# Kernel tuning notes

Hardware: AMD Instinct MI355X
Metric: run time of the kernel (lower is better)

## Reference

```python
import jax, jax.numpy as jnp
import numpy as np

BATCH, SEQ_LEN, D_MODEL, STATE_DIM = 8, 4096, 512, 64
LN_EPS = 1e-5


def _hippo_log_neg_eigs(state_dim):
    A = np.zeros((state_dim, state_dim))
    for i in range(state_dim):
        for j in range(state_dim):
            if i > j:
                A[i, j] = -((2 * i + 1) ** 0.5) * ((2 * j + 1) ** 0.5)
            elif i == j:
                A[i, j] = -(i + 1)
    ev = np.sort(np.linalg.eigvals(A).real)[:state_dim]
    return np.log(-ev + 1e-06).astype(np.float32)


def setup_inputs() -> dict:
    key = jax.random.key(0)
    ks = jax.random.split(key, 8)
    d, s = D_MODEL, STATE_DIM
    return {
        "x": jax.random.normal(ks[0], (BATCH, SEQ_LEN, d), dtype=jnp.float32),
        "log_A": jnp.asarray(_hippo_log_neg_eigs(s)),
        "B": jax.random.normal(ks[1], (d, s), dtype=jnp.float32) * 0.01,
        "C": jax.random.normal(ks[2], (s, d), dtype=jnp.float32) * 0.01,
        "D": jnp.zeros((d,), dtype=jnp.float32),
        "log_dt": jnp.zeros((), dtype=jnp.float32),
        "gamma": jnp.ones((d,), dtype=jnp.float32),
        "beta": jnp.zeros((d,), dtype=jnp.float32),
        "W1": jax.random.normal(ks[3], (d, 2 * d), dtype=jnp.float32) * (1.0 / np.sqrt(d)),
        "b1": jnp.zeros((2 * d,), dtype=jnp.float32),
        "W2": jax.random.normal(ks[4], (2 * d, d), dtype=jnp.float32) * (1.0 / np.sqrt(2 * d)),
        "b2": jnp.zeros((d,), dtype=jnp.float32),
    }


def _layernorm(x, gamma, beta):
    mu = jnp.mean(x, axis=-1, keepdims=True)
    var = jnp.mean(jnp.square(x - mu), axis=-1, keepdims=True)
    return (x - mu) * jax.lax.rsqrt(var + LN_EPS) * gamma + beta


def reference(x, log_A, B, C, D, log_dt, gamma, beta, W1, b1, W2, b2):
    residual = x
    xn = _layernorm(x, gamma, beta)  # [B, L, D]

    dt = jnp.exp(log_dt)
    A_bar = jnp.exp(-jnp.exp(log_A) * dt)  # [S]

    # Precompute input projections for all timesteps, then scan the diagonal recurrence.
    xB = jnp.einsum("bld,ds->lbs", xn, B)  # [L, B, S]
    h0 = jnp.zeros((xn.shape[0], A_bar.shape[0]), dtype=xn.dtype)

    def step(h, xb_t):
        h = A_bar * h + xb_t
        return h, h

    _, hs = jax.lax.scan(step, h0, xB)  # hs: [L, B, S]

    y = jnp.einsum("lbs,sd->bld", hs, C) + xn * D  # [B, L, D]
    y = y + residual

    yn = _layernorm(y, gamma, beta)
    mlp = jax.nn.gelu(yn @ W1 + b1, approximate=False) @ W2 + b2
    return y + mlp
```

## Files before the change

kernel.cpp:

```cpp
#include <hip/hip_runtime.h>
#include <math.h>

#define BATCH 8
#define SEQL 4096
#define DMODEL 512
#define SDIM 64
#define MROWS (BATCH * SEQL)
#define LN_EPS 1e-5f

typedef __attribute__((ext_vector_type(8))) short bf16x8;
typedef __attribute__((ext_vector_type(4))) float f32x4;

__device__ __forceinline__ float wave_sum(float v) {
#pragma unroll
  for (int off = 32; off > 0; off >>= 1) v += __shfl_xor(v, off, 64);
  return v;
}

__device__ __forceinline__ unsigned short f2bf(float f) {
  unsigned int u = __float_as_uint(f);
  u += 0x7fffu + ((u >> 16) & 1u);
  return (unsigned short)(u >> 16);
}

__device__ __forceinline__ float gelu_fast(float v) {
  float s = v * 0.70710678118654752f;
  float ax = fabsf(s);
  float t = 1.0f / (1.0f + 0.3275911f * ax);
  float p = ((((1.061405429f * t - 1.453152027f) * t + 1.421413741f) * t - 0.284496736f) * t +
             0.254829592f) *
            t;
  float er = 1.0f - p * __expf(-ax * ax);
  er = copysignf(er, s);
  return 0.5f * v * (1.0f + er);
}

__device__ __forceinline__ void gl2lds16(const void* g, void* l) {
  __builtin_amdgcn_global_load_lds((const __attribute__((address_space(1))) void*)g,
                                   (__attribute__((address_space(3))) void*)l, 16, 0, 0);
}

__global__ void ln_stats_kernel(const float* __restrict__ x, float* __restrict__ mu,
                                float* __restrict__ rstd, unsigned short* __restrict__ xbf) {
  int row = blockIdx.x * 4 + (threadIdx.x >> 6);
  int lane = threadIdx.x & 63;
  const float4* xp = (const float4*)(x + (size_t)row * DMODEL);
  float4 a = xp[lane * 2];
  float4 b = xp[lane * 2 + 1];
  float s = a.x + a.y + a.z + a.w + b.x + b.y + b.z + b.w;
  float q = a.x * a.x + a.y * a.y + a.z * a.z + a.w * a.w + b.x * b.x + b.y * b.y +
            b.z * b.z + b.w * b.w;
  s = wave_sum(s);
  q = wave_sum(q);
  uint4 pk;
  pk.x = (unsigned)f2bf(a.x) | ((unsigned)f2bf(a.y) << 16);
  pk.y = (unsigned)f2bf(a.z) | ((unsigned)f2bf(a.w) << 16);
  pk.z = (unsigned)f2bf(b.x) | ((unsigned)f2bf(b.y) << 16);
  pk.w = (unsigned)f2bf(b.z) | ((unsigned)f2bf(b.w) << 16);
  ((uint4*)(xbf + (size_t)row * DMODEL))[lane] = pk;
  if (lane == 0) {
    float m = s * (1.0f / DMODEL);
    float var = q * (1.0f / DMODEL) - m * m;
    mu[row] = m;
    rstd[row] = rsqrtf(var + LN_EPS);
  }
}

__device__ __forceinline__ void transpose_body(const float* __restrict__ W,
                                               unsigned short* __restrict__ Wt, int K, int N,
                                               int bx, int by,
                                               unsigned short (*tile)[65]) {
  int k0 = by * 64, n0 = bx * 64;
  int tx = threadIdx.x & 15, ty = threadIdx.x >> 4;
#pragma unroll
  for (int p = 0; p < 4; ++p) {
    int k = p * 16 + ty;
    float4 v = *(const float4*)&W[(size_t)(k0 + k) * N + n0 + tx * 4];
    tile[tx * 4 + 0][k] = f2bf(v.x);
    tile[tx * 4 + 1][k] = f2bf(v.y);
    tile[tx * 4 + 2][k] = f2bf(v.z);
    tile[tx * 4 + 3][k] = f2bf(v.w);
  }
  __syncthreads();
#pragma unroll
  for (int p = 0; p < 4; ++p) {
    int n = p * 16 + ty;
    ushort4 o;
    o.x = tile[n][tx * 4 + 0];
    o.y = tile[n][tx * 4 + 1];
    o.z = tile[n][tx * 4 + 2];
    o.w = tile[n][tx * 4 + 3];
    *(ushort4*)&Wt[(size_t)(n0 + n) * K + k0 + tx * 4] = o;
  }
}

__global__ __launch_bounds__(256) void prep_all_kernel(
    const float* __restrict__ W1, const float* __restrict__ W2, const float* __restrict__ Cm,
    const float* __restrict__ Bm, const float* __restrict__ gamma,
    const float* __restrict__ beta, unsigned short* __restrict__ w1t,
    unsigned short* __restrict__ w2t, unsigned short* __restrict__ ctb,
    unsigned short* __restrict__ Bgt, float* __restrict__ gB, float* __restrict__ bB) {
  __shared__ unsigned short tile[64][65];
  int b = blockIdx.x;
  if (b < 128) {
    transpose_body(W1, w1t, 512, 1024, b & 15, b >> 4, tile);
  } else if (b < 256) {
    transpose_body(W2, w2t, 1024, 512, (b - 128) & 7, (b - 128) >> 3, tile);
  } else if (b < 264) {
    transpose_body(Cm, ctb, 64, 512, b - 256, 0, tile);
  } else {
    int s = (b - 264) * 4 + (threadIdx.x >> 6);
    int l = threadIdx.x & 63;
    float gs = 0.0f, bs = 0.0f;
    unsigned short tmp[8];
#pragma unroll
    for (int u = 0; u < 8; ++u) {
      int d = l * 8 + u;
      float bv = Bm[(size_t)d * SDIM + s];
      float gv = gamma[d], ev = beta[d];
      gs += gv * bv;
      bs += ev * bv;
      tmp[u] = f2bf(gv * bv);
    }
    *(ushort4*)&Bgt[(size_t)s * DMODEL + l * 8] = make_ushort4(tmp[0], tmp[1], tmp[2], tmp[3]);
    *(ushort4*)&Bgt[(size_t)s * DMODEL + l * 8 + 4] =
        make_ushort4(tmp[4], tmp[5], tmp[6], tmp[7]);
    gs = wave_sum(gs);
    bs = wave_sum(bs);
    if (l == 0) {
      gB[s] = gs;
      bB[s] = bs;
    }
  }
}

__global__ __launch_bounds__(256) void xb_mfma_kernel(
    const unsigned short* __restrict__ xbf, const unsigned short* __restrict__ Bgt,
    const float* __restrict__ mu, const float* __restrict__ rstd, const float* __restrict__ gB,
    const float* __restrict__ bB, float* __restrict__ xB) {
  __shared__ unsigned short As[128 * 32];
  __shared__ unsigned short Bs[64 * 32];
  const int t = threadIdx.x;
  const int wave = t >> 6, lane = t & 63;
  const int m0 = blockIdx.x * 128;
  const int wm = wave * 32;
  const int row = t >> 2, seg = t & 3;
  const int fr = lane & 15, fq = lane >> 4;
  f32x4 acc[2][4] = {};
  for (int k0 = 0; k0 < DMODEL; k0 += 32) {
    __syncthreads();
    gl2lds16(xbf + (size_t)(m0 + row) * DMODEL + k0 + seg * 8, As + (size_t)(wave * 16) * 32);
    gl2lds16(xbf + (size_t)(m0 + 64 + row) * DMODEL + k0 + seg * 8,
             As + (size_t)(64 + wave * 16) * 32);
    gl2lds16(Bgt + (size_t)row * DMODEL + k0 + seg * 8, Bs + (size_t)(wave * 16) * 32);
    __syncthreads();
#pragma unroll
    for (int i = 0; i < 2; ++i) {
      bf16x8 a = *(const bf16x8*)&As[(wm + i * 16 + fr) * 32 + fq * 8];
#pragma unroll
      for (int j = 0; j < 4; ++j) {
        bf16x8 b = *(const bf16x8*)&Bs[(j * 16 + fr) * 32 + fq * 8];
        acc[i][j] = __builtin_amdgcn_mfma_f32_16x16x32_bf16(a, b, acc[i][j], 0, 0, 0);
      }
    }
  }
#pragma unroll
  for (int i = 0; i < 2; ++i)
#pragma unroll
    for (int r = 0; r < 4; ++r) {
      const int m = m0 + wm + i * 16 + fq * 4 + r;
      const float rr = rstd[m], negmurr = -mu[m] * rstd[m];
#pragma unroll
      for (int j = 0; j < 4; ++j) {
        const int s = j * 16 + fr;
        xB[(size_t)m * SDIM + s] = rr * acc[i][j][r] + negmurr * gB[s] + bB[s];
      }
    }
}

__global__ void scan_ends_kernel(const float* __restrict__ xB, const float* __restrict__ logA,
                                 const float* __restrict__ logdt, float* __restrict__ ends) {
  int t = blockIdx.x * 256 + threadIdx.x;
  int s = t & 63;
  int c = (t >> 6) & 63;
  int b = t >> 12;
  float a = expf(-expf(logA[s]) * expf(logdt[0]));
  const float* p = xB + ((size_t)(b * SEQL + c * 64)) * SDIM + s;
  float e = 0.0f;
#pragma unroll
  for (int i = 0; i < 64; ++i) e = a * e + p[(size_t)i * SDIM];
  ends[(b * 64 + c) * 64 + s] = e;
}

__global__ void scan_fix_kernel(const float* __restrict__ logA, const float* __restrict__ logdt,
                                const float* __restrict__ ends, const float* __restrict__ xB,
                                unsigned short* __restrict__ hsb) {
  int t = blockIdx.x * 256 + threadIdx.x;
  int s = t & 63;
  int c = (t >> 6) & 63;
  int b = t >> 12;
  float a = expf(-expf(logA[s]) * expf(logdt[0]));
  float a64 = a;
#pragma unroll
  for (int i = 0; i < 6; ++i) a64 *= a64;
  float h = 0.0f;
  for (int cp = 0; cp < c; ++cp) h = a64 * h + ends[(b * 64 + cp) * 64 + s];
  const float* p = xB + ((size_t)(b * SEQL + c * 64)) * SDIM + s;
  unsigned short* q = hsb + ((size_t)(b * SEQL + c * 64)) * SDIM + s;
#pragma unroll
  for (int i = 0; i < 64; ++i) {
    h = a * h + p[(size_t)i * SDIM];
    q[(size_t)i * SDIM] = f2bf(h);
  }
}

__global__ __launch_bounds__(256) void y_gemm_mfma_kernel(
    const unsigned short* __restrict__ hsb, const unsigned short* __restrict__ ctb,
    const float* __restrict__ x, const float* __restrict__ mu1,
    const float* __restrict__ rstd1, const float* __restrict__ gamma,
    const float* __restrict__ beta, const float* __restrict__ Dv, float* __restrict__ out) {
  __shared__ unsigned short As[2 * 128 * 32];
  __shared__ unsigned short Bs[2 * 128 * 32];
  const int t = threadIdx.x;
  const int w = t >> 6, lane = t & 63;
  const int m0 = blockIdx.y * 128, n0 = blockIdx.x * 128;
  const int wm = (w >> 1) * 64, wn = (w & 1) * 64;
  const int fr = lane & 15, fq = lane >> 4;
  const int srow = t >> 2, sseg = t & 3;
#pragma unroll
  for (int h = 0; h < 2; ++h)
#pragma unroll
    for (int c = 0; c < 2; ++c) {
      gl2lds16(hsb + (size_t)(m0 + c * 64 + srow) * SDIM + h * 32 + sseg * 8,
               As + ((size_t)h * 128 + c * 64 + w * 16) * 32);
      gl2lds16(ctb + (size_t)(n0 + c * 64 + srow) * SDIM + h * 32 + sseg * 8,
               Bs + ((size_t)h * 128 + c * 64 + w * 16) * 32);
    }
  __syncthreads();
  f32x4 acc[4][4] = {};
#pragma unroll
  for (int h = 0; h < 2; ++h) {
    bf16x8 a[4], b[4];
#pragma unroll
    for (int i = 0; i < 4; ++i)
      a[i] = *(const bf16x8*)&As[((size_t)h * 128 + wm + i * 16 + fr) * 32 + fq * 8];
#pragma unroll
    for (int j = 0; j < 4; ++j)
      b[j] = *(const bf16x8*)&Bs[((size_t)h * 128 + wn + j * 16 + fr) * 32 + fq * 8];
#pragma unroll
    for (int i = 0; i < 4; ++i)
#pragma unroll
      for (int j = 0; j < 4; ++j)
        acc[i][j] = __builtin_amdgcn_mfma_f32_16x16x32_bf16(a[i], b[j], acc[i][j], 0, 0, 0);
  }
  float mm[4][4], rr[4][4];
#pragma unroll
  for (int i = 0; i < 4; ++i)
#pragma unroll
    for (int r = 0; r < 4; ++r) {
      int m = m0 + wm + i * 16 + fq * 4 + r;
      mm[i][r] = mu1[m];
      rr[i][r] = rstd1[m];
    }
#pragma unroll
  for (int j = 0; j < 4; ++j) {
    const int n = n0 + wn + j * 16 + fr;
    const float ga = gamma[n], be = beta[n], dd = Dv[n];
#pragma unroll
    for (int i = 0; i < 4; ++i) {
      float xv[4];
#pragma unroll
      for (int r = 0; r < 4; ++r)
        xv[r] = x[(size_t)(m0 + wm + i * 16 + fq * 4 + r) * DMODEL + n];
#pragma unroll
      for (int r = 0; r < 4; ++r) {
        float yv = acc[i][j][r] + ((xv[r] - mm[i][r]) * rr[i][r] * ga + be) * dd + xv[r];
        out[(size_t)(m0 + wm + i * 16 + fq * 4 + r) * DMODEL + n] = yv;
      }
    }
  }
}

__global__ void ln_apply_kernel(const float* __restrict__ y, const float* __restrict__ gamma,
                                const float* __restrict__ beta,
                                unsigned short* __restrict__ yn) {
  int row = blockIdx.x * 4 + (threadIdx.x >> 6);
  int lane = threadIdx.x & 63;
  const float4* yp = (const float4*)(y + (size_t)row * DMODEL);
  float4 a = yp[lane * 2];
  float4 b = yp[lane * 2 + 1];
  float s = a.x + a.y + a.z + a.w + b.x + b.y + b.z + b.w;
  float q = a.x * a.x + a.y * a.y + a.z * a.z + a.w * a.w + b.x * b.x + b.y * b.y +
            b.z * b.z + b.w * b.w;
  s = wave_sum(s);
  q = wave_sum(q);
  float m = s * (1.0f / DMODEL);
  float var = q * (1.0f / DMODEL) - m * m;
  float rs = rsqrtf(var + LN_EPS);
  const float4* gp = (const float4*)gamma;
  const float4* bp = (const float4*)beta;
  float4 g0 = gp[lane * 2], g1 = gp[lane * 2 + 1];
  float4 e0 = bp[lane * 2], e1 = bp[lane * 2 + 1];
  float o0x = (a.x - m) * rs * g0.x + e0.x, o0y = (a.y - m) * rs * g0.y + e0.y;
  float o0z = (a.z - m) * rs * g0.z + e0.z, o0w = (a.w - m) * rs * g0.w + e0.w;
  float o1x = (b.x - m) * rs * g1.x + e1.x, o1y = (b.y - m) * rs * g1.y + e1.y;
  float o1z = (b.z - m) * rs * g1.z + e1.z, o1w = (b.w - m) * rs * g1.w + e1.w;
  uint4 pk;
  pk.x = (unsigned)f2bf(o0x) | ((unsigned)f2bf(o0y) << 16);
  pk.y = (unsigned)f2bf(o0z) | ((unsigned)f2bf(o0w) << 16);
  pk.z = (unsigned)f2bf(o1x) | ((unsigned)f2bf(o1y) << 16);
  pk.w = (unsigned)f2bf(o1z) | ((unsigned)f2bf(o1w) << 16);
  ((uint4*)(yn + (size_t)row * DMODEL))[lane] = pk;
}

template <int K, int NALL, int EPI>
__global__ __launch_bounds__(512, 2) void gemm256_kernel(
    const unsigned short* __restrict__ Am, const unsigned short* __restrict__ Bm,
    const float* __restrict__ bias, unsigned short* __restrict__ gout,
    float* __restrict__ out) {
  __shared__ alignas(16) unsigned short As[2][256 * 64];
  __shared__ alignas(16) unsigned short Bs[2][256 * 64];
  const int t = threadIdx.x;
  const int wid = t >> 6, lane = t & 63;
  const int m0 = blockIdx.y * 256, n0 = blockIdx.x * 256;
  const int wm = (wid >> 2) * 128, wn = (wid & 3) * 64;
  const int fr = lane & 15, fq = lane >> 4;
  constexpr int NT = K / 64;
  const int srow = t >> 3;
  const int ksw = ((t & 7) ^ ((t >> 3) & 7)) << 3;

  auto stageA = [&](int bb, int h, int kt) {
    const unsigned short* s0 = Am + (size_t)(m0 + h * 128 + srow) * K + kt * 64 + ksw;
    gl2lds16(s0, &As[bb][(h * 128 + wid * 8) * 64]);
    gl2lds16(s0 + (size_t)64 * K, &As[bb][(h * 128 + 64 + wid * 8) * 64]);
  };
  auto stageB = [&](int bb, int h, int kt) {
    const unsigned short* s0 = Bm + (size_t)(n0 + h * 128 + srow) * K + kt * 64 + ksw;
    gl2lds16(s0, &Bs[bb][(h * 128 + wid * 8) * 64]);
    gl2lds16(s0 + (size_t)64 * K, &Bs[bb][(h * 128 + 64 + wid * 8) * 64]);
  };
  auto LDA = [&](int bb, int i, int s) -> bf16x8 {
    const int row = wm + i * 16 + fr;
    const int slot = (s * 4 + fq) ^ (fr & 7);
    return *(const bf16x8*)&As[bb][row * 64 + slot * 8];
  };
  auto LDB = [&](int bb, int j, int s) -> bf16x8 {
    const int col = wn + j * 16 + fr;
    const int slot = (s * 4 + fq) ^ (fr & 7);
    return *(const bf16x8*)&Bs[bb][col * 64 + slot * 8];
  };

  stageA(0, 0, 0);
  stageA(0, 1, 0);
  stageB(0, 0, 0);
  stageB(0, 1, 0);
  stageB(1, 0, 1);
  stageB(1, 1, 1);
  asm volatile("s_waitcnt vmcnt(4)" ::: "memory");
  asm volatile("s_barrier" ::: "memory");

  f32x4 acc[8][4] = {};
  for (int c = 0; c < NT; ++c) {
    const int b = c & 1;
    bf16x8 bfr[2][4];
#pragma unroll
    for (int q = 0; q < 4; ++q) {
      bf16x8 a2[2][2];
#pragma unroll
      for (int ii = 0; ii < 2; ++ii)
#pragma unroll
        for (int s = 0; s < 2; ++s) a2[ii][s] = LDA(b, 2 * q + ii, s);
      if (q == 0) {
#pragma unroll
        for (int s = 0; s < 2; ++s)
#pragma unroll
          for (int j = 0; j < 4; ++j) bfr[s][j] = LDB(b, j, s);
        if (c + 1 < NT) stageA(b ^ 1, 0, c + 1);
      } else if (q == 1) {
        if (c + 1 < NT) stageA(b ^ 1, 1, c + 1);
      } else if (q == 2) {
        asm volatile("" ::: "memory");
        if (c + 2 < NT) stageB(b, 0, c + 2);
      } else {
        if (c + 2 < NT) stageB(b, 1, c + 2);
      }
      asm volatile("s_barrier" ::: "memory");
      __builtin_amdgcn_s_setprio(1);
#pragma unroll
      for (int ii = 0; ii < 2; ++ii)
#pragma unroll
        for (int s = 0; s < 2; ++s)
#pragma unroll
          for (int j = 0; j < 4; ++j)
            acc[2 * q + ii][j] = __builtin_amdgcn_mfma_f32_16x16x32_bf16(
                a2[ii][s], bfr[s][j], acc[2 * q + ii][j], 0, 0, 0);
      __builtin_amdgcn_s_setprio(0);
      if (q < 3) {
        asm volatile("s_barrier" ::: "memory");
      } else if (c < NT - 1) {
        if (c < NT - 2)
          asm volatile("s_waitcnt vmcnt(4)" ::: "memory");
        else
          asm volatile("s_waitcnt vmcnt(0)" ::: "memory");
        asm volatile("s_barrier" ::: "memory");
      }
    }
  }

#pragma unroll
  for (int i = 0; i < 8; ++i)
#pragma unroll
    for (int j = 0; j < 4; ++j) {
      const int cg = n0 + wn + j * 16 + fr;
      const float bb = bias[cg];
#pragma unroll
      for (int r = 0; r < 4; ++r) {
        const int rg = m0 + wm + i * 16 + fq * 4 + r;
        if (EPI == 0) {
          gout[(size_t)rg * NALL + cg] = f2bf(gelu_fast(acc[i][j][r] + bb));
        } else {
          const size_t off = (size_t)rg * NALL + cg;
          out[off] = out[off] + acc[i][j][r] + bb;
        }
      }
    }
}

extern "C" void kernel_launch(void* const* d_in, const int* in_sizes, int n_in, void* d_out,
                              int out_size, void* d_ws, size_t ws_size, hipStream_t stream) {
  const float* x = (const float*)d_in[0];
  const float* logA = (const float*)d_in[1];
  const float* Bm = (const float*)d_in[2];
  const float* Cm = (const float*)d_in[3];
  const float* Dv = (const float*)d_in[4];
  const float* logdt = (const float*)d_in[5];
  const float* gamma = (const float*)d_in[6];
  const float* beta = (const float*)d_in[7];
  const float* W1 = (const float*)d_in[8];
  const float* b1 = (const float*)d_in[9];
  const float* W2 = (const float*)d_in[10];
  const float* b2 = (const float*)d_in[11];
  float* out = (float*)d_out;

  char* ws = (char*)d_ws;
  float* mu1 = (float*)(ws + 0);
  float* rstd1 = (float*)(ws + 131072);
  float* ends = (float*)(ws + 262144);
  float* gB = (float*)(ws + 524288);
  float* bB = (float*)(ws + 524800);
  unsigned short* Bgt = (unsigned short*)(ws + 525312);
  unsigned short* ctb = (unsigned short*)(ws + 590848);
  unsigned short* w1t = (unsigned short*)(ws + 656384);
  unsigned short* w2t = (unsigned short*)(ws + 1704960);
  unsigned short* g = (unsigned short*)(ws + 2753536);
  unsigned short* xbf = (unsigned short*)(ws + 2753536);
  float* xB = (float*)(ws + 69862400);
  unsigned short* hsb = (unsigned short*)(ws + 78251008);
  unsigned short* yn = (unsigned short*)(ws + 82445312);

  prep_all_kernel<<<280, 256, 0, stream>>>(W1, W2, Cm, Bm, gamma, beta, w1t, w2t, ctb, Bgt, gB,
                                           bB);
  ln_stats_kernel<<<MROWS / 4, 256, 0, stream>>>(x, mu1, rstd1, xbf);
  xb_mfma_kernel<<<MROWS / 128, 256, 0, stream>>>(xbf, Bgt, mu1, rstd1, gB, bB, xB);
  scan_ends_kernel<<<128, 256, 0, stream>>>(xB, logA, logdt, ends);
  scan_fix_kernel<<<128, 256, 0, stream>>>(logA, logdt, ends, xB, hsb);
  y_gemm_mfma_kernel<<<dim3(DMODEL / 128, MROWS / 128), 256, 0, stream>>>(
      hsb, ctb, x, mu1, rstd1, gamma, beta, Dv, out);
  ln_apply_kernel<<<MROWS / 4, 256, 0, stream>>>(out, gamma, beta, yn);
  gemm256_kernel<512, 1024, 0><<<dim3(1024 / 256, MROWS / 256), 512, 0, stream>>>(
      yn, w1t, b1, g, nullptr);
  gemm256_kernel<1024, 512, 1><<<dim3(512 / 256, MROWS / 256), 512, 0, stream>>>(
      g, w2t, b2, nullptr, out);
}
```

Baseline: 322.3 us.

## Use inline-asm LDS reads with precomputed addresses and swizzle GEMM workgroup order

```diff
diff --git a/kernel.cpp b/kernel.cpp
--- a/kernel.cpp
+++ b/kernel.cpp
@@ -10,6 +10,7 @@
 
 typedef __attribute__((ext_vector_type(8))) short bf16x8;
 typedef __attribute__((ext_vector_type(4))) float f32x4;
+typedef __attribute__((ext_vector_type(4))) int i32x4;
 
 __device__ __forceinline__ float wave_sum(float v) {
 #pragma unroll
@@ -38,6 +39,21 @@
 __device__ __forceinline__ void gl2lds16(const void* g, void* l) {
   __builtin_amdgcn_global_load_lds((const __attribute__((address_space(1))) void*)g,
                                    (__attribute__((address_space(3))) void*)l, 16, 0, 0);
+}
+
+__device__ __forceinline__ unsigned lds_addr(const void* p) {
+  return (unsigned)(uintptr_t)(__attribute__((address_space(3))) const void*)p;
+}
+
+__device__ __forceinline__ bf16x8 ldsr128(unsigned addr) {
+  i32x4 r;
+  asm volatile("ds_read_b128 %0, %1" : "=v"(r) : "v"(addr));
+  union {
+    i32x4 i;
+    bf16x8 h;
+  } u;
+  u.i = r;
+  return u.h;
 }
 
 __global__ void ln_stats_kernel(const float* __restrict__ x, float* __restrict__ mu,
@@ -322,7 +338,10 @@
   __shared__ alignas(16) unsigned short Bs[2][256 * 64];
   const int t = threadIdx.x;
   const int wid = t >> 6, lane = t & 63;
-  const int m0 = blockIdx.y * 256, n0 = blockIdx.x * 256;
+  const int nwg = gridDim.x * gridDim.y;
+  const int orig = blockIdx.y * gridDim.x + blockIdx.x;
+  const int swz = (orig & 7) * (nwg >> 3) + (orig >> 3);
+  const int m0 = (swz / gridDim.x) * 256, n0 = (swz % gridDim.x) * 256;
   const int wm = (wid >> 2) * 128, wn = (wid & 3) * 64;
   const int fr = lane & 15, fq = lane >> 4;
   constexpr int NT = K / 64;
@@ -339,16 +358,13 @@
     gl2lds16(s0, &Bs[bb][(h * 128 + wid * 8) * 64]);
     gl2lds16(s0 + (size_t)64 * K, &Bs[bb][(h * 128 + 64 + wid * 8) * 64]);
   };
-  auto LDA = [&](int bb, int i, int s) -> bf16x8 {
-    const int row = wm + i * 16 + fr;
-    const int slot = (s * 4 + fq) ^ (fr & 7);
-    return *(const bf16x8*)&As[bb][row * 64 + slot * 8];
-  };
-  auto LDB = [&](int bb, int j, int s) -> bf16x8 {
-    const int col = wn + j * 16 + fr;
-    const int slot = (s * 4 + fq) ^ (fr & 7);
-    return *(const bf16x8*)&Bs[bb][col * 64 + slot * 8];
-  };
+
+  const unsigned aA0 = lds_addr(&As[0][0]) + (unsigned)((wm + fr) * 128 + (fq ^ (fr & 7)) * 16);
+  const unsigned aA1 =
+      lds_addr(&As[0][0]) + (unsigned)((wm + fr) * 128 + ((4 + fq) ^ (fr & 7)) * 16);
+  const unsigned aB0 = lds_addr(&Bs[0][0]) + (unsigned)((wn + fr) * 128 + (fq ^ (fr & 7)) * 16);
+  const unsigned aB1 =
+      lds_addr(&Bs[0][0]) + (unsigned)((wn + fr) * 128 + ((4 + fq) ^ (fr & 7)) * 16);
 
   stageA(0, 0, 0);
   stageA(0, 1, 0);
@@ -357,34 +373,37 @@
   stageB(1, 0, 1);
   stageB(1, 1, 1);
   asm volatile("s_waitcnt vmcnt(4)" ::: "memory");
-  asm volatile("s_barrier" ::: "memory");
+  __builtin_amdgcn_s_barrier();
 
   f32x4 acc[8][4] = {};
   for (int c = 0; c < NT; ++c) {
     const int b = c & 1;
+    const unsigned bo = (unsigned)(b * 32768);
     bf16x8 bfr[2][4];
 #pragma unroll
     for (int q = 0; q < 4; ++q) {
       bf16x8 a2[2][2];
-#pragma unroll
-      for (int ii = 0; ii < 2; ++ii)
-#pragma unroll
-        for (int s = 0; s < 2; ++s) a2[ii][s] = LDA(b, 2 * q + ii, s);
+      a2[0][0] = ldsr128(aA0 + bo + (2 * q) * 2048);
+      a2[0][1] = ldsr128(aA1 + bo + (2 * q) * 2048);
+      a2[1][0] = ldsr128(aA0 + bo + (2 * q + 1) * 2048);
+      a2[1][1] = ldsr128(aA1 + bo + (2 * q + 1) * 2048);
       if (q == 0) {
 #pragma unroll
-        for (int s = 0; s < 2; ++s)
-#pragma unroll
-          for (int j = 0; j < 4; ++j) bfr[s][j] = LDB(b, j, s);
+        for (int j = 0; j < 4; ++j) {
+          bfr[0][j] = ldsr128(aB0 + bo + j * 2048);
+          bfr[1][j] = ldsr128(aB1 + bo + j * 2048);
+        }
         if (c + 1 < NT) stageA(b ^ 1, 0, c + 1);
       } else if (q == 1) {
         if (c + 1 < NT) stageA(b ^ 1, 1, c + 1);
       } else if (q == 2) {
-        asm volatile("" ::: "memory");
         if (c + 2 < NT) stageB(b, 0, c + 2);
       } else {
         if (c + 2 < NT) stageB(b, 1, c + 2);
       }
-      asm volatile("s_barrier" ::: "memory");
+      __builtin_amdgcn_s_barrier();
+      asm volatile("s_waitcnt lgkmcnt(0)" ::: "memory");
+      __builtin_amdgcn_sched_barrier(0);
       __builtin_amdgcn_s_setprio(1);
 #pragma unroll
       for (int ii = 0; ii < 2; ++ii)
@@ -396,13 +415,13 @@
                 a2[ii][s], bfr[s][j], acc[2 * q + ii][j], 0, 0, 0);
       __builtin_amdgcn_s_setprio(0);
       if (q < 3) {
-        asm volatile("s_barrier" ::: "memory");
+        __builtin_amdgcn_s_barrier();
       } else if (c < NT - 1) {
         if (c < NT - 2)
           asm volatile("s_waitcnt vmcnt(4)" ::: "memory");
         else
           asm volatile("s_waitcnt vmcnt(0)" ::: "memory");
-        asm volatile("s_barrier" ::: "memory");
+        __builtin_amdgcn_s_barrier();
       }
     }
   }
```

New measurement: 318.4 us. About the same (-1.2%).
